# Kernel optimization log

Measured on AMD Instinct MI355X. Metric: run time of the kernel, lower is better.

Reference implementation:

```python
import jax, jax.numpy as jnp
import numpy as np

# dims: E=2 experts, R=64 lora rank, IN=768, HID=3072, OUT=768, B=32, S=1280 (chunks 256+1024)
SCALE = 128.0 / 64.0  # lora_alpha / lora_rank


def setup_inputs() -> dict:
    key = jax.random.key(0)
    ks = jax.random.split(key, 9)
    B, S, IN, HID, OUT, E, R = 32, 1280, 768, 3072, 768, 2, 64
    inp = {
        "x": jax.random.normal(ks[0], (B, S, IN), jnp.float32),
        "w1": jax.random.normal(ks[1], (HID, IN), jnp.float32) * 0.02,
        "bias1": jax.random.normal(ks[2], (HID,), jnp.float32) * 0.02,
        "a1": jax.random.normal(ks[3], (E, R, IN), jnp.float32) * 0.02,
        "b1": jax.random.normal(ks[4], (E, HID, R), jnp.float32) * 0.02,
        "w2": jax.random.normal(ks[5], (OUT, HID), jnp.float32) * 0.02,
        "bias2": jax.random.normal(ks[6], (OUT,), jnp.float32) * 0.02,
        "a2": jax.random.normal(ks[7], (E, R, HID), jnp.float32) * 0.02,
        "b2": jax.random.normal(ks[8], (E, OUT, R), jnp.float32) * 0.02,
        "expert_indices": np.array([0, 1], dtype=np.int64),
        "chunk_sizes": np.array([256, 1024], dtype=np.int64),
    }
    return inp


def _lora_linear(x, w, bias, a_e, b_e):
    # y = x @ W^T + b + scale * (x @ A^T) @ B^T   (LoRA, dropout=0)
    return x @ w.T + bias + SCALE * ((x @ a_e.T) @ b_e.T)


def reference(x, w1, bias1, a1, b1, w2, bias2, a2, b2, expert_indices, chunk_sizes):
    sizes = [int(s) for s in np.asarray(chunk_sizes)]
    eids = [int(e) for e in np.asarray(expert_indices)]
    outs = []
    start = 0
    for sz, e in zip(sizes, eids):
        xc = x[:, start:start + sz]  # [B, sz, IN] static slice
        start += sz
        h = _lora_linear(xc, w1, bias1, a1[e], b1[e])
        h = jax.nn.gelu(h, approximate=False)  # nn.GELU default (erf)
        y = _lora_linear(h, w2, bias2, a2[e], b2[e])
        outs.append(y)
    return jnp.concatenate(outs, axis=1)
```

## Files before the change

### kernel.cpp

```cpp
#include <hip/hip_runtime.h>

typedef __attribute__((ext_vector_type(8))) short short8;
typedef __attribute__((ext_vector_type(4))) float f32x4;

__device__ __forceinline__ unsigned short f2bf(float f) {
  union { float f; unsigned u; } v; v.f = f;
  unsigned r = v.u + 0x7fffu + ((v.u >> 16) & 1u);
  return (unsigned short)(r >> 16);
}

__device__ __forceinline__ void async16(const void* g, void* l) {
  __builtin_amdgcn_global_load_lds(
      (const __attribute__((address_space(1))) unsigned*)g,
      (__attribute__((address_space(3))) unsigned*)l, 16, 0, 0);
}

#define BARRIER() __builtin_amdgcn_s_barrier()
#define LGKM0()                                                     \
  do {                                                              \
    asm volatile("s_waitcnt lgkmcnt(0)" ::: "memory");              \
    __builtin_amdgcn_sched_barrier(0);                              \
  } while (0)
#define WAIT_VM(N) asm volatile("s_waitcnt vmcnt(" #N ")" ::: "memory")

__global__ void cvt_bf16_kernel(const float4* __restrict__ in,
                                ushort4* __restrict__ out, int n4) {
  int i = blockIdx.x * blockDim.x + threadIdx.x;
  int stride = gridDim.x * blockDim.x;
  for (; i < n4; i += stride) {
    float4 v = in[i];
    ushort4 o;
    o.x = f2bf(v.x); o.y = f2bf(v.y); o.z = f2bf(v.z); o.w = f2bf(v.w);
    out[i] = o;
  }
}

__global__ void make_weff(const float* __restrict__ w,
                          const float* __restrict__ bmat,
                          const float* __restrict__ amat,
                          unsigned short* __restrict__ out,
                          int J, int K) {
  const int e = blockIdx.y;
  const float* a = amat + (size_t)e * 64 * K;
  const float* b = bmat + (size_t)e * J * 64;
  const int j0 = blockIdx.x * 16;
  __shared__ float bs[16][64];
  const int tid = threadIdx.x;
  for (int i = tid; i < 16 * 64; i += 256)
    bs[i >> 6][i & 63] = b[(size_t)(j0 + (i >> 6)) * 64 + (i & 63)];
  __syncthreads();
  for (int k = tid; k < K; k += 256) {
    float acc[16];
#pragma unroll
    for (int jj = 0; jj < 16; ++jj) acc[jj] = 0.f;
    for (int r = 0; r < 64; ++r) {
      float av = a[(size_t)r * K + k];
#pragma unroll
      for (int jj = 0; jj < 16; ++jj) acc[jj] += bs[jj][r] * av;
    }
#pragma unroll
    for (int jj = 0; jj < 16; ++jj) {
      float v = w[(size_t)(j0 + jj) * K + k] + 2.0f * acc[jj];
      out[((size_t)e * J + j0 + jj) * K + k] = f2bf(v);
    }
  }
}


#define STAGE(Xp, Xs, half, t)                                                 \
  do {                                                                         \
    const unsigned short* _g =                                                 \
        (Xp) + (size_t)((half) * 128) * K + (size_t)(t) * 64 + gstep;          \
    unsigned short* _l = (Xs) + (half) * 8192 + loff;                          \
    async16(_g, _l);                                                           \
    async16(_g + (size_t)64 * K, _l + 4096);                                   \
  } while (0)

#define RDA(Xs, mbase)                                                         \
  _Pragma("unroll") for (int m_ = 0; m_ < 4; ++m_)                             \
  _Pragma("unroll") for (int kk_ = 0; kk_ < 2; ++kk_)                          \
      afm[m_][kk_] = *(const short8*)((const char*)(Xs) +                      \
                                      ((mbase) >> 2) * 16384 + arowB +         \
                                      m_ * 2048 + cb[kk_]);

#define RDB(Xs, nbase)                                                         \
  _Pragma("unroll") for (int n_ = 0; n_ < 2; ++n_)                             \
  _Pragma("unroll") for (int kk_ = 0; kk_ < 2; ++kk_)                          \
      bfv[(nbase) + n_][kk_] = *(const short8*)((const char*)(Xs) +            \
                                                ((nbase) >> 1) * 16384 +       \
                                                browB + n_ * 2048 + cb[kk_]);

#define MFMAQ(mbase, nbase)                                                    \
  __builtin_amdgcn_s_setprio(1);                                               \
  _Pragma("unroll") for (int m_ = 0; m_ < 4; ++m_)                             \
  _Pragma("unroll") for (int n_ = 0; n_ < 2; ++n_)                             \
  _Pragma("unroll") for (int kk_ = 0; kk_ < 2; ++kk_)                          \
      acc[(mbase) + m_][(nbase) + n_] =                                        \
          __builtin_amdgcn_mfma_f32_16x16x32_bf16(                             \
              afm[m_][kk_], bfv[(nbase) + n_][kk_],                            \
              acc[(mbase) + m_][(nbase) + n_], 0, 0, 0);                       \
  __builtin_amdgcn_s_setprio(0);

template <bool FUSE_GELU, bool OUT_BF16>
__global__ __launch_bounds__(512, 2) void gemm256(
    const unsigned short* __restrict__ A, const unsigned short* __restrict__ Bw,
    const float* __restrict__ bias, void* __restrict__ Cout, int N, int K,
    int NXT) {
  extern __shared__ unsigned short lds[];
  unsigned short* As0 = lds;
  unsigned short* As1 = lds + 16384;
  unsigned short* Bs0 = lds + 32768;
  unsigned short* Bs1 = lds + 49152;

  const int tid = threadIdx.x;
  const int w = tid >> 6, lane = tid & 63;

  const int nwg = gridDim.x, bid = blockIdx.x;
  const int qchunk = nwg >> 3;
  const int wg = (bid & 7) * qchunk + (bid >> 3);
  const int by = wg / NXT, bx = wg - by * NXT;
  const int m0 = by << 8, n0 = bx << 8;
  const int e = (m0 % 1280) ? 1 : 0;
  const unsigned short* Ap = A + (size_t)m0 * K;
  const unsigned short* Bp = Bw + ((size_t)e * N + n0) * K;

  const int wr = w >> 2, wc = w & 3;
  const int fr = lane & 15;
  const int swz = (fr & 7) << 4;
  const int cb[2] = {(((lane >> 4) << 4) + 0) ^ swz,
                     (((lane >> 4) << 4) + 64) ^ swz};
  const int arowB = (wr * 64 + fr) * 128;
  const int browB = (wc * 32 + fr) * 128;

  const int rql = lane >> 3;
  const int c16 = (lane & 7) ^ rql;
  const size_t gstep = (size_t)(w * 8 + rql) * K + c16 * 8;
  const int loff = w * 512;

  f32x4 acc[8][4] = {};
  short8 afm[4][2];
  short8 bfv[4][2];

  const int T = K >> 6;
  const int niter = T >> 1;

  STAGE(Ap, As0, 0, 0); STAGE(Ap, As0, 1, 0);
  STAGE(Bp, Bs0, 0, 0); STAGE(Bp, Bs0, 1, 0);
  STAGE(Ap, As1, 0, 1);
  STAGE(Bp, Bs1, 0, 1); STAGE(Bp, Bs1, 1, 1);
  WAIT_VM(6);
  BARRIER();

  for (int i = 0; i < niter; ++i) {
    const int t1 = 2 * i + 1;
    int u2 = 2 * i + 2; if (u2 >= T) u2 -= T;
    int u3 = 2 * i + 3; if (u3 >= T) u3 -= T;

    RDA(As0, 0); RDB(Bs0, 0);
    STAGE(Ap, As1, 1, t1);
    BARRIER(); LGKM0();
    MFMAQ(0, 0);
    BARRIER();
    RDB(Bs0, 2);
    STAGE(Ap, As0, 0, u2);
    BARRIER(); LGKM0();
    MFMAQ(0, 2);
    BARRIER();
    RDA(As0, 4);
    STAGE(Bp, Bs0, 0, u2);
    BARRIER(); LGKM0();
    MFMAQ(4, 0);
    BARRIER();
    STAGE(Bp, Bs0, 1, u2);
    BARRIER();
    MFMAQ(4, 2);
    WAIT_VM(6);
    BARRIER();
    RDA(As1, 0); RDB(Bs1, 0);
    STAGE(Ap, As0, 1, u2);
    BARRIER(); LGKM0();
    MFMAQ(0, 0);
    BARRIER();
    RDB(Bs1, 2);
    STAGE(Ap, As1, 0, u3);
    BARRIER(); LGKM0();
    MFMAQ(0, 2);
    BARRIER();
    RDA(As1, 4);
    STAGE(Bp, Bs1, 0, u3);
    BARRIER(); LGKM0();
    MFMAQ(4, 0);
    BARRIER();
    STAGE(Bp, Bs1, 1, u3);
    BARRIER();
    MFMAQ(4, 2);
    WAIT_VM(6);
    BARRIER();
  }

  const int lrow = (lane >> 4) << 2;
#pragma unroll
  for (int mi = 0; mi < 8; ++mi) {
    const int rbase = m0 + ((mi >> 2) << 7) + wr * 64 + ((mi & 3) << 4) + lrow;
#pragma unroll
    for (int n = 0; n < 4; ++n) {
      const int col = n0 + ((n >> 1) << 7) + wc * 32 + ((n & 1) << 4) + fr;
      const float bv = bias[col];
#pragma unroll
      for (int j = 0; j < 4; ++j) {
        const int row = rbase + j;
        float v = acc[mi][n][j] + bv;
        if (FUSE_GELU) v = 0.5f * v * (1.0f + erff(v * 0.70710678118f));
        if (OUT_BF16)
          ((unsigned short*)Cout)[(size_t)row * N + col] = f2bf(v);
        else
          ((float*)Cout)[(size_t)row * N + col] = v;
      }
    }
  }
}

extern "C" void kernel_launch(void* const* d_in, const int* in_sizes, int n_in,
                              void* d_out, int out_size, void* d_ws,
                              size_t ws_size, hipStream_t stream) {
  const float* x = (const float*)d_in[0];
  const float* w1 = (const float*)d_in[1];
  const float* bias1 = (const float*)d_in[2];
  const float* a1 = (const float*)d_in[3];
  const float* b1 = (const float*)d_in[4];
  const float* w2 = (const float*)d_in[5];
  const float* bias2 = (const float*)d_in[6];
  const float* a2 = (const float*)d_in[7];
  const float* b2 = (const float*)d_in[8];
  float* out = (float*)d_out;

  char* ws = (char*)d_ws;
  unsigned short* x_bf = (unsigned short*)(ws + 0);
  unsigned short* w1e = (unsigned short*)(ws + 62914560);
  unsigned short* w2e = (unsigned short*)(ws + 72351744);
  unsigned short* h = (unsigned short*)(ws + 81788928);

  hipFuncSetAttribute(reinterpret_cast<const void*>(&gemm256<true, true>),
                      hipFuncAttributeMaxDynamicSharedMemorySize, 131072);
  hipFuncSetAttribute(reinterpret_cast<const void*>(&gemm256<false, false>),
                      hipFuncAttributeMaxDynamicSharedMemorySize, 131072);

  cvt_bf16_kernel<<<4096, 256, 0, stream>>>((const float4*)x, (ushort4*)x_bf,
                                            40960 * 768 / 4);
  make_weff<<<dim3(3072 / 16, 2), 256, 0, stream>>>(w1, b1, a1, w1e, 3072, 768);
  make_weff<<<dim3(768 / 16, 2), 256, 0, stream>>>(w2, b2, a2, w2e, 768, 3072);

  gemm256<true, true><<<1920, 512, 131072, stream>>>(x_bf, w1e, bias1, h, 3072,
                                                     768, 12);
  gemm256<false, false><<<480, 512, 131072, stream>>>(h, w2e, bias2, out, 768,
                                                      3072, 3);
}
```

Measured before the change: 742.3 us.

## Double-buffer MFMA fragments with ping-pong registers and replace erff with polynomial GELU

Restructures the GEMM main loop so that LDS fragment reads for the next quarter-tile go into a second register set while MFMAs consume the current one. This removes the explicit lgkmcnt(0) waits and halves the barriers per phase. Global staging offsets are now precomputed byte offsets that are incremented each iteration. The exact erff in the GELU epilogue is replaced by an Abramowitz-Stegun polynomial with __expf, which is cheaper but only accurate to about 1e-7 absolute. The new schedule relies on the compiler inserting the correct LDS waits, and the extra fragment registers add register pressure.

```diff
diff --git a/kernel.cpp b/kernel.cpp
--- a/kernel.cpp
+++ b/kernel.cpp
@@ -15,13 +15,22 @@
       (__attribute__((address_space(3))) unsigned*)l, 16, 0, 0);
 }
 
+#define SBAR() __builtin_amdgcn_sched_barrier(0)
+#define MEMFENCE() asm volatile("" ::: "memory")
 #define BARRIER() __builtin_amdgcn_s_barrier()
-#define LGKM0()                                                     \
-  do {                                                              \
-    asm volatile("s_waitcnt lgkmcnt(0)" ::: "memory");              \
-    __builtin_amdgcn_sched_barrier(0);                              \
-  } while (0)
 #define WAIT_VM(N) asm volatile("s_waitcnt vmcnt(" #N ")" ::: "memory")
+
+__device__ __forceinline__ float gelu_exact(float v) {
+  float s = v * 0.70710678118f;
+  float x = fabsf(s);
+  float t = 1.0f / (1.0f + 0.3275911f * x);
+  float p = t * (0.254829592f +
+            t * (-0.284496736f +
+            t * (1.421413741f + t * (-1.453152027f + t * 1.061405429f))));
+  float er = 1.0f - p * __expf(-x * x);
+  er = copysignf(er, s);
+  return 0.5f * v * (1.0f + er);
+}
 
 __global__ void cvt_bf16_kernel(const float4* __restrict__ in,
                                 ushort4* __restrict__ out, int n4) {
@@ -67,39 +76,40 @@
 }
 
 
-#define STAGE(Xp, Xs, half, t)                                                 \
+#define STAGE(Xp, Xs, half, ob)                                                \
   do {                                                                         \
-    const unsigned short* _g =                                                 \
-        (Xp) + (size_t)((half) * 128) * K + (size_t)(t) * 64 + gstep;          \
+    const char* _g = (const char*)((Xp) + (size_t)((half) * 128) * K) +        \
+                     gbyte + (ob);                                             \
     unsigned short* _l = (Xs) + (half) * 8192 + loff;                          \
     async16(_g, _l);                                                           \
-    async16(_g + (size_t)64 * K, _l + 4096);                                   \
+    async16(_g + (size_t)K * 128, _l + 4096);                                  \
   } while (0)
 
-#define RDA(Xs, mbase)                                                         \
+#define RDA_TO(dst, Xs, hoff)                                                  \
   _Pragma("unroll") for (int m_ = 0; m_ < 4; ++m_)                             \
   _Pragma("unroll") for (int kk_ = 0; kk_ < 2; ++kk_)                          \
-      afm[m_][kk_] = *(const short8*)((const char*)(Xs) +                      \
-                                      ((mbase) >> 2) * 16384 + arowB +         \
-                                      m_ * 2048 + cb[kk_]);
-
-#define RDB(Xs, nbase)                                                         \
+      dst[m_][kk_] = *(const short8*)((const char*)(Xs) + (hoff) * 16384 +     \
+                                      arowB + m_ * 2048 + cb[kk_]);
+
+#define RDB_TO(dst, Xs, hoff)                                                  \
   _Pragma("unroll") for (int n_ = 0; n_ < 2; ++n_)                             \
   _Pragma("unroll") for (int kk_ = 0; kk_ < 2; ++kk_)                          \
-      bfv[(nbase) + n_][kk_] = *(const short8*)((const char*)(Xs) +            \
-                                                ((nbase) >> 1) * 16384 +       \
-                                                browB + n_ * 2048 + cb[kk_]);
-
-#define MFMAQ(mbase, nbase)                                                    \
+      dst[n_][kk_] = *(const short8*)((const char*)(Xs) + (hoff) * 16384 +     \
+                                      browB + n_ * 2048 + cb[kk_]);
+
+#define MFMAQ(af, bf, mbase, nbase)                                            \
   __builtin_amdgcn_s_setprio(1);                                               \
   _Pragma("unroll") for (int m_ = 0; m_ < 4; ++m_)                             \
   _Pragma("unroll") for (int n_ = 0; n_ < 2; ++n_)                             \
   _Pragma("unroll") for (int kk_ = 0; kk_ < 2; ++kk_)                          \
       acc[(mbase) + m_][(nbase) + n_] =                                        \
           __builtin_amdgcn_mfma_f32_16x16x32_bf16(                             \
-              afm[m_][kk_], bfv[(nbase) + n_][kk_],                            \
+              af[m_][kk_], bf[n_][kk_],                                        \
               acc[(mbase) + m_][(nbase) + n_], 0, 0, 0);                       \
   __builtin_amdgcn_s_setprio(0);
+
+#define PHASE_END()                                                            \
+  do { SBAR(); MEMFENCE(); BARRIER(); SBAR(); MEMFENCE(); } while (0)
 
 template <bool FUSE_GELU, bool OUT_BF16>
 __global__ __launch_bounds__(512, 2) void gemm256(
@@ -134,68 +144,75 @@
 
   const int rql = lane >> 3;
   const int c16 = (lane & 7) ^ rql;
-  const size_t gstep = (size_t)(w * 8 + rql) * K + c16 * 8;
+  const size_t gbyte = ((size_t)(w * 8 + rql) * K + c16 * 8) * 2;
   const int loff = w * 512;
 
   f32x4 acc[8][4] = {};
-  short8 afm[4][2];
-  short8 bfv[4][2];
+  short8 afmX[4][2], afmY[4][2];
+  short8 bfvX[2][2], bfvY[2][2];
 
   const int T = K >> 6;
   const int niter = T >> 1;
-
-  STAGE(Ap, As0, 0, 0); STAGE(Ap, As0, 1, 0);
-  STAGE(Bp, Bs0, 0, 0); STAGE(Bp, Bs0, 1, 0);
-  STAGE(Ap, As1, 0, 1);
-  STAGE(Bp, Bs1, 0, 1); STAGE(Bp, Bs1, 1, 1);
-  WAIT_VM(6);
-  BARRIER();
+  const int KB2 = K << 1;
+
+  STAGE(Ap, As0, 0, 0); STAGE(Bp, Bs0, 0, 0);
+  STAGE(Ap, As0, 1, 0); STAGE(Bp, Bs0, 1, 0);
+  STAGE(Ap, As1, 0, 128); STAGE(Bp, Bs1, 0, 128);
+  SBAR(); WAIT_VM(4); SBAR();
+  MEMFENCE(); BARRIER(); SBAR(); MEMFENCE();
+  RDA_TO(afmX, As0, 0); RDB_TO(bfvX, Bs0, 0);
+
+  int ob1 = 128, ob2 = 256, ob3 = 384;
+  if (ob2 >= KB2) ob2 -= KB2;
+  if (ob3 >= KB2) ob3 -= KB2;
 
   for (int i = 0; i < niter; ++i) {
-    const int t1 = 2 * i + 1;
-    int u2 = 2 * i + 2; if (u2 >= T) u2 -= T;
-    int u3 = 2 * i + 3; if (u3 >= T) u3 -= T;
-
-    RDA(As0, 0); RDB(Bs0, 0);
-    STAGE(Ap, As1, 1, t1);
-    BARRIER(); LGKM0();
-    MFMAQ(0, 0);
-    BARRIER();
-    RDB(Bs0, 2);
-    STAGE(Ap, As0, 0, u2);
-    BARRIER(); LGKM0();
-    MFMAQ(0, 2);
-    BARRIER();
-    RDA(As0, 4);
-    STAGE(Bp, Bs0, 0, u2);
-    BARRIER(); LGKM0();
-    MFMAQ(4, 0);
-    BARRIER();
-    STAGE(Bp, Bs0, 1, u2);
-    BARRIER();
-    MFMAQ(4, 2);
-    WAIT_VM(6);
-    BARRIER();
-    RDA(As1, 0); RDB(Bs1, 0);
-    STAGE(Ap, As0, 1, u2);
-    BARRIER(); LGKM0();
-    MFMAQ(0, 0);
-    BARRIER();
-    RDB(Bs1, 2);
-    STAGE(Ap, As1, 0, u3);
-    BARRIER(); LGKM0();
-    MFMAQ(0, 2);
-    BARRIER();
-    RDA(As1, 4);
-    STAGE(Bp, Bs1, 0, u3);
-    BARRIER(); LGKM0();
-    MFMAQ(4, 0);
-    BARRIER();
-    STAGE(Bp, Bs1, 1, u3);
-    BARRIER();
-    MFMAQ(4, 2);
-    WAIT_VM(6);
-    BARRIER();
+    RDB_TO(bfvY, Bs0, 1);
+    STAGE(Ap, As1, 1, ob1);
+    SBAR();
+    MFMAQ(afmX, bfvX, 0, 0);
+    PHASE_END();
+    RDA_TO(afmY, As0, 1);
+    STAGE(Bp, Bs1, 1, ob1);
+    SBAR();
+    MFMAQ(afmX, bfvY, 0, 2);
+    PHASE_END();
+    STAGE(Ap, As0, 0, ob2);
+    SBAR();
+    MFMAQ(afmY, bfvX, 4, 0);
+    SBAR(); WAIT_VM(6);
+    PHASE_END();
+    RDA_TO(afmX, As1, 0); RDB_TO(bfvX, Bs1, 0);
+    STAGE(Bp, Bs0, 0, ob2);
+    SBAR();
+    MFMAQ(afmY, bfvY, 4, 2);
+    SBAR(); WAIT_VM(4);
+    PHASE_END();
+    RDB_TO(bfvY, Bs1, 1);
+    STAGE(Ap, As0, 1, ob2);
+    SBAR();
+    MFMAQ(afmX, bfvX, 0, 0);
+    PHASE_END();
+    RDA_TO(afmY, As1, 1);
+    STAGE(Bp, Bs0, 1, ob2);
+    SBAR();
+    MFMAQ(afmX, bfvY, 0, 2);
+    PHASE_END();
+    STAGE(Ap, As1, 0, ob3);
+    SBAR();
+    MFMAQ(afmY, bfvX, 4, 0);
+    SBAR(); WAIT_VM(6);
+    PHASE_END();
+    RDA_TO(afmX, As0, 0); RDB_TO(bfvX, Bs0, 0);
+    STAGE(Bp, Bs1, 0, ob3);
+    SBAR();
+    MFMAQ(afmY, bfvY, 4, 2);
+    SBAR(); WAIT_VM(4);
+    PHASE_END();
+
+    ob1 += 256; if (ob1 >= KB2) ob1 -= KB2;
+    ob2 += 256; if (ob2 >= KB2) ob2 -= KB2;
+    ob3 += 256; if (ob3 >= KB2) ob3 -= KB2;
   }
 
   const int lrow = (lane >> 4) << 2;
@@ -210,7 +227,7 @@
       for (int j = 0; j < 4; ++j) {
         const int row = rbase + j;
         float v = acc[mi][n][j] + bv;
-        if (FUSE_GELU) v = 0.5f * v * (1.0f + erff(v * 0.70710678118f));
+        if (FUSE_GELU) v = gelu_exact(v);
         if (OUT_BF16)
           ((unsigned short*)Cout)[(size_t)row * N + col] = f2bf(v);
         else
```

Result: faster. 713.8 us (-3.8%).
